# Kernel tuning notes

Hardware: AMD Instinct MI355X
Metric: run time of the kernel (lower is better)

## Reference

```python
import jax, jax.numpy as jnp
import numpy as np

H, D, E, C, F = 12, 64, 768, 512, 3072  # heads, kq_dim, emb_dim, context_dim, mlp_hid
EPS = 1e-5
SCALE = 1.0 / float(np.sqrt(D))


def setup_inputs() -> dict:
    key = jax.random.key(0)
    ks = jax.random.split(key, 12)
    rn = lambda k, s: jax.random.normal(k, s, dtype=jnp.float32) * 0.02
    z = lambda s: jnp.zeros(s, jnp.float32)
    o = lambda s: jnp.ones(s, jnp.float32)
    return {
        "emb": jax.random.normal(ks[0], (8, 1024, E), dtype=jnp.float32),
        "context": jax.random.normal(ks[1], (8, 256, C), dtype=jnp.float32),
        # self-attention (qkv_bias=False, value_up has bias)
        "sa_wq": rn(ks[2], (E, H * D)), "sa_wk": rn(ks[3], (E, H * D)),
        "sa_wv": rn(ks[4], (E, H * D)), "sa_wo": rn(ks[5], (H * D, E)), "sa_wo_b": z((E,)),
        "sa_qn_g": o((D,)), "sa_qn_b": z((D,)), "sa_kn_g": o((D,)), "sa_kn_b": z((D,)),
        # cross-attention
        "ca_wq": rn(ks[6], (E, H * D)), "ca_wk": rn(ks[7], (C, H * D)),
        "ca_wv": rn(ks[8], (C, H * D)), "ca_wo": rn(ks[9], (H * D, E)), "ca_wo_b": z((E,)),
        "ca_qn_g": o((D,)), "ca_qn_b": z((D,)), "ca_kn_g": o((D,)), "ca_kn_b": z((D,)),
        # MLP
        "mlp_w1": rn(ks[10], (E, F)), "mlp_b1": z((F,)),
        "mlp_w2": rn(ks[11], (F, E)), "mlp_b2": z((E,)),
        # block LayerNorms
        "ln1_g": o((E,)), "ln1_b": z((E,)),
        "ln2_g": o((E,)), "ln2_b": z((E,)),
        "ln3_g": o((E,)), "ln3_b": z((E,)),
    }


def _ln(x, g, b):
    m = jnp.mean(x, axis=-1, keepdims=True)
    v = jnp.mean(jnp.square(x - m), axis=-1, keepdims=True)
    return (x - m) / jnp.sqrt(v + EPS) * g + b


def _heads(x):  # [B,S,H*D] -> [B,H,S,D]
    B, S = x.shape[:2]
    return x.reshape(B, S, H, D).transpose(0, 2, 1, 3)


def _merge(x):  # [B,H,S,D] -> [B,S,H*D]
    B, h, S, d = x.shape
    return x.transpose(0, 2, 1, 3).reshape(B, S, h * d)


def _attn(qx, kvx, wq, wk, wv, wo, wo_b, qg, qb, kg, kb):
    q = _ln(_heads(qx @ wq), qg, qb)   # per-head QK-LayerNorm
    k = _ln(_heads(kvx @ wk), kg, kb)
    v = _heads(kvx @ wv)
    a = jax.nn.softmax(jnp.einsum('bhqd,bhkd->bhqk', q, k) * SCALE, axis=-1)
    return _merge(jnp.einsum('bhqk,bhkd->bhqd', a, v)) @ wo + wo_b


def reference(emb, context,
              sa_wq, sa_wk, sa_wv, sa_wo, sa_wo_b, sa_qn_g, sa_qn_b, sa_kn_g, sa_kn_b,
              ca_wq, ca_wk, ca_wv, ca_wo, ca_wo_b, ca_qn_g, ca_qn_b, ca_kn_g, ca_kn_b,
              mlp_w1, mlp_b1, mlp_w2, mlp_b2,
              ln1_g, ln1_b, ln2_g, ln2_b, ln3_g, ln3_b):
    # MultiHeadAttention.forward returns value + emb, and the block adds emb again
    sa = _attn(emb, emb, sa_wq, sa_wk, sa_wv, sa_wo, sa_wo_b,
               sa_qn_g, sa_qn_b, sa_kn_g, sa_kn_b)
    x = _ln(sa + emb + emb, ln1_g, ln1_b)  # faithful double residual
    ca = _attn(x, context, ca_wq, ca_wk, ca_wv, ca_wo, ca_wo_b,
               ca_qn_g, ca_qn_b, ca_kn_g, ca_kn_b)
    x = _ln(x + ca, ln2_g, ln2_b)
    x = jax.nn.gelu(x @ mlp_w1 + mlp_b1, approximate=False) @ mlp_w2 + mlp_b2
    return _ln(x, ln3_g, ln3_b)  # note: no residual around MLP in the original
```

## Files before the change

kernel.cpp:

```cpp
#include <hip/hip_runtime.h>
#include <hip/hip_bf16.h>
#include <math.h>

#define NH 12
#define HD 64
#define ED 768
#define CD 512
#define FD 3072
#define BB 8
#define SS 1024
#define TT 256
#define LN_EPS 1e-5f
#define ATT_SCALE 0.125f
#define QSC_LOG2E 0.1803368801111204f
#define P_M0 11.55f
#define TOT_R 6291456

typedef __attribute__((ext_vector_type(8))) __bf16 bf16x8;
typedef __attribute__((ext_vector_type(4))) __bf16 bf16x4;
typedef __attribute__((ext_vector_type(4))) float f32x4;

typedef const __attribute__((address_space(1))) void* gas1_t;
typedef __attribute__((address_space(3))) void* las3_t;

__device__ __forceinline__ void gl16(const void* g, void* l) {
  __builtin_amdgcn_global_load_lds((gas1_t)g, (las3_t)l, 16, 0, 0);
}

__device__ __forceinline__ ushort f2bf(float f) {
  union { __bf16 b; ushort u; } c;
  c.b = (__bf16)f;
  return c.u;
}
__device__ __forceinline__ float bf2f(ushort u) {
  return __uint_as_float((unsigned)u << 16);
}

__device__ __forceinline__ float gelu_fast(float c) {
  const float x2 = c * c;
  const float ex = __builtin_amdgcn_exp2f(c * (-2.3022084f - 0.10294325f * x2));
  return c * __builtin_amdgcn_rcpf(1.0f + ex);
}

__device__ __forceinline__ bf16x8 frag64(const ushort (*T)[64], int row, int q8) {
  return *(const bf16x8*)((const char*)T + row * 128 + ((q8 ^ (row & 7)) << 4));
}

struct CvtPack {
  const float* src[12];
  ushort* dst[12];
  int kd[12];
  int nd[12];
  int off[13];
};

__global__ __launch_bounds__(256) void cvt_all(CvtPack P) {
  __shared__ float t[32][33];
  const int flat = blockIdx.x;
  int j = 0;
  while (j < 11 && flat >= P.off[j + 1]) ++j;
  const int rel = flat - P.off[j];
  if (P.nd[j] == 0) {
    const int i = rel * 256 + threadIdx.x;
    if (i < P.kd[j]) {
      float4 v = ((const float4*)P.src[j])[i];
      ((ushort4*)P.dst[j])[i] =
          make_ushort4(f2bf(v.x), f2bf(v.y), f2bf(v.z), f2bf(v.w));
    }
    return;
  }
  const int Kd = P.kd[j], Nd = P.nd[j];
  const int ntx = Nd >> 5;
  const int n0 = (rel % ntx) * 32, k0 = (rel / ntx) * 32;
  const float* W = P.src[j];
  ushort* WT = P.dst[j];
  const int tx = threadIdx.x & 31, ty = threadIdx.x >> 5;
#pragma unroll
  for (int r = 0; r < 4; ++r)
    t[ty + 8 * r][tx] = W[(size_t)(k0 + ty + 8 * r) * Nd + n0 + tx];
  __syncthreads();
#pragma unroll
  for (int r = 0; r < 4; ++r)
    WT[(size_t)(n0 + ty + 8 * r) * Kd + k0 + tx] = f2bf(t[tx][ty + 8 * r]);
}

template <int MODE>
__global__ __launch_bounds__(256) void mfma_gemm(
    const ushort* __restrict__ A, const ushort* __restrict__ Wt,
    const float* __restrict__ bias, void* __restrict__ outp,
    int M, int N, int K, int sshift,
    const float* __restrict__ qg, const float* __restrict__ qb,
    const float* __restrict__ kg, const float* __restrict__ kb,
    int t_q, int t_k, int t_v) {
  __shared__ ushort As[2][128][64];
  __shared__ ushort Bs[2][128][64];
  const int tid = threadIdx.x;
  const int m0 = blockIdx.x * 128, n0 = blockIdx.y * 128;
  const int lane = tid & 63;
  const int wr = ((tid >> 6) >> 1) * 64, wc = ((tid >> 6) & 1) * 64;
  const int l15 = lane & 15, g = lane >> 4;
  f32x4 acc[4][4] = {};

  auto stage = [&](int bi, int kt) {
#pragma unroll
    for (int p = 0; p < 4; ++p) {
      const int flat = p * 256 + tid;
      const int row = flat >> 3, q8 = flat & 7;
      const int kc = 8 * (q8 ^ (row & 7));
      gl16(&A[(size_t)(m0 + row) * K + kt + kc], (char*)As[bi] + flat * 16);
      gl16(&Wt[(size_t)(n0 + row) * K + kt + kc], (char*)Bs[bi] + flat * 16);
    }
  };

  stage(0, 0);
  __syncthreads();
  int cur = 0;
  for (int kt = 0; kt < K; kt += 64) {
    if (kt + 64 < K) stage(cur ^ 1, kt + 64);
#pragma unroll
    for (int h = 0; h < 2; ++h) {
      bf16x8 af[4], bfv[4];
#pragma unroll
      for (int i = 0; i < 4; ++i) {
        af[i] = frag64(As[cur], wr + i * 16 + l15, 4 * h + g);
        bfv[i] = frag64(Bs[cur], wc + i * 16 + l15, 4 * h + g);
      }
#pragma unroll
      for (int i = 0; i < 4; ++i)
#pragma unroll
        for (int j = 0; j < 4; ++j)
          acc[i][j] = __builtin_amdgcn_mfma_f32_16x16x32_bf16(af[i], bfv[j],
                                                              acc[i][j], 0, 0, 0);
    }
    __syncthreads();
    cur ^= 1;
  }

  if (MODE == 2) {
    ushort* out = (ushort*)outp;
    const int Stok = 1 << sshift, smask = Stok - 1;
    const int ht0 = (n0 + wc) >> 6;
    const int t = ht0 / NH, h = ht0 - t * NH;
    const bool isq = (t == t_q), isk = (t == t_k);
    if (isq || isk) {
      const float* gg = isq ? qg : kg;
      const float* bb = isq ? qb : kb;
      const float osc = isq ? QSC_LOG2E : 1.0f;
      float gv[4], bv[4];
#pragma unroll
      for (int j = 0; j < 4; ++j) {
        gv[j] = gg[j * 16 + l15];
        bv[j] = bb[j * 16 + l15];
      }
#pragma unroll
      for (int i = 0; i < 4; ++i)
#pragma unroll
        for (int r = 0; r < 4; ++r) {
          float s = acc[i][0][r] + acc[i][1][r] + acc[i][2][r] + acc[i][3][r];
          float sq = acc[i][0][r] * acc[i][0][r] + acc[i][1][r] * acc[i][1][r] +
                     acc[i][2][r] * acc[i][2][r] + acc[i][3][r] * acc[i][3][r];
          s += __shfl_xor(s, 1);  sq += __shfl_xor(sq, 1);
          s += __shfl_xor(s, 2);  sq += __shfl_xor(sq, 2);
          s += __shfl_xor(s, 4);  sq += __shfl_xor(sq, 4);
          s += __shfl_xor(s, 8);  sq += __shfl_xor(sq, 8);
          const float mean = s * (1.0f / 64.0f);
          const float var = sq * (1.0f / 64.0f) - mean * mean;
          const float rs = rsqrtf(fmaxf(var, 0.0f) + LN_EPS);
#pragma unroll
          for (int j = 0; j < 4; ++j)
            acc[i][j][r] = ((acc[i][j][r] - mean) * rs * gv[j] + bv[j]) * osc;
        }
    }
    if (t == t_v) {
#pragma unroll
      for (int i = 0; i < 4; ++i) {
        const int row = m0 + wr + i * 16 + g * 4;
        const int b = row >> sshift, s2 = row & smask;
        ushort* obase =
            out + (size_t)t * TOT_R + (((size_t)b * NH + h) * 64) * Stok + s2;
#pragma unroll
        for (int j = 0; j < 4; ++j) {
          const int d = j * 16 + l15;
          ushort4 pk = make_ushort4(f2bf(acc[i][j][0]), f2bf(acc[i][j][1]),
                                    f2bf(acc[i][j][2]), f2bf(acc[i][j][3]));
          *(ushort4*)&obase[(size_t)d * Stok] = pk;
        }
      }
    } else {
#pragma unroll
      for (int i = 0; i < 4; ++i)
#pragma unroll
        for (int r = 0; r < 4; ++r) {
          const int row = m0 + wr + i * 16 + g * 4 + r;
          const int b = row >> sshift, s2 = row & smask;
          ushort* orow =
              out + (size_t)t * TOT_R + (((size_t)b * NH + h) * Stok + s2) * 64;
#pragma unroll
          for (int j = 0; j < 4; ++j) orow[j * 16 + l15] = f2bf(acc[i][j][r]);
        }
    }
  } else {
#pragma unroll
    for (int i = 0; i < 4; ++i) {
#pragma unroll
      for (int j = 0; j < 4; ++j) {
        const int gc = n0 + wc + j * 16 + l15;
        const float bv = bias ? bias[gc] : 0.0f;
#pragma unroll
        for (int r = 0; r < 4; ++r) {
          const int row = m0 + wr + i * 16 + g * 4 + r;
          float c = acc[i][j][r] + bv;
          if (MODE == 1) {
            c = gelu_fast(c);
            ((ushort*)outp)[(size_t)row * N + gc] = f2bf(c);
          } else if (MODE == 3) {
            ((ushort*)outp)[(size_t)row * N + gc] = f2bf(c);
          } else {
            ((float*)outp)[(size_t)row * N + gc] = c;
          }
        }
      }
    }
  }
}

__global__ __launch_bounds__(256) void mfma_gemm_ca(
    const ushort* __restrict__ A0, const ushort* __restrict__ Wt0,
    void* __restrict__ out0,
    const ushort* __restrict__ A1, const ushort* __restrict__ Wt1,
    void* __restrict__ out1,
    const float* __restrict__ qg, const float* __restrict__ qb,
    const float* __restrict__ kg, const float* __restrict__ kb) {
  __shared__ ushort As[2][128][64];
  __shared__ ushort Bs[2][128][64];
  const int tid = threadIdx.x;
  const int fb = blockIdx.x;
  const ushort* A;
  const ushort* Wt;
  ushort* out;
  int m0, n0, K, sshift, t_q, t_k, t_v;
  if (fb < 192) {
    A = A1; Wt = Wt1; out = (ushort*)out1;
    K = CD; sshift = 8;
    m0 = (fb & 15) * 128; n0 = (fb >> 4) * 128;
    t_q = -1; t_k = 0; t_v = 1;
  } else {
    const int id = fb - 192;
    A = A0; Wt = Wt0; out = (ushort*)out0;
    K = ED; sshift = 10;
    m0 = (id & 63) * 128; n0 = (id >> 6) * 128;
    t_q = 0; t_k = -1; t_v = -1;
  }
  const int lane = tid & 63;
  const int wr = ((tid >> 6) >> 1) * 64, wc = ((tid >> 6) & 1) * 64;
  const int l15 = lane & 15, g = lane >> 4;
  f32x4 acc[4][4] = {};

  auto stage = [&](int bi, int kt) {
#pragma unroll
    for (int p = 0; p < 4; ++p) {
      const int flat = p * 256 + tid;
      const int row = flat >> 3, q8 = flat & 7;
      const int kc = 8 * (q8 ^ (row & 7));
      gl16(&A[(size_t)(m0 + row) * K + kt + kc], (char*)As[bi] + flat * 16);
      gl16(&Wt[(size_t)(n0 + row) * K + kt + kc], (char*)Bs[bi] + flat * 16);
    }
  };

  stage(0, 0);
  __syncthreads();
  int cur = 0;
  for (int kt = 0; kt < K; kt += 64) {
    if (kt + 64 < K) stage(cur ^ 1, kt + 64);
#pragma unroll
    for (int h = 0; h < 2; ++h) {
      bf16x8 af[4], bfv[4];
#pragma unroll
      for (int i = 0; i < 4; ++i) {
        af[i] = frag64(As[cur], wr + i * 16 + l15, 4 * h + g);
        bfv[i] = frag64(Bs[cur], wc + i * 16 + l15, 4 * h + g);
      }
#pragma unroll
      for (int i = 0; i < 4; ++i)
#pragma unroll
        for (int j = 0; j < 4; ++j)
          acc[i][j] = __builtin_amdgcn_mfma_f32_16x16x32_bf16(af[i], bfv[j],
                                                              acc[i][j], 0, 0, 0);
    }
    __syncthreads();
    cur ^= 1;
  }

  const int Stok = 1 << sshift, smask = Stok - 1;
  const int ht0 = (n0 + wc) >> 6;
  const int t = ht0 / NH, h = ht0 - t * NH;
  const bool isq = (t == t_q), isk = (t == t_k);
  if (isq || isk) {
    const float* gg = isq ? qg : kg;
    const float* bb = isq ? qb : kb;
    const float osc = isq ? QSC_LOG2E : 1.0f;
    float gv[4], bv[4];
#pragma unroll
    for (int j = 0; j < 4; ++j) {
      gv[j] = gg[j * 16 + l15];
      bv[j] = bb[j * 16 + l15];
    }
#pragma unroll
    for (int i = 0; i < 4; ++i)
#pragma unroll
      for (int r = 0; r < 4; ++r) {
        float s = acc[i][0][r] + acc[i][1][r] + acc[i][2][r] + acc[i][3][r];
        float sq = acc[i][0][r] * acc[i][0][r] + acc[i][1][r] * acc[i][1][r] +
                   acc[i][2][r] * acc[i][2][r] + acc[i][3][r] * acc[i][3][r];
        s += __shfl_xor(s, 1);  sq += __shfl_xor(sq, 1);
        s += __shfl_xor(s, 2);  sq += __shfl_xor(sq, 2);
        s += __shfl_xor(s, 4);  sq += __shfl_xor(sq, 4);
        s += __shfl_xor(s, 8);  sq += __shfl_xor(sq, 8);
        const float mean = s * (1.0f / 64.0f);
        const float var = sq * (1.0f / 64.0f) - mean * mean;
        const float rs = rsqrtf(fmaxf(var, 0.0f) + LN_EPS);
#pragma unroll
        for (int j = 0; j < 4; ++j)
          acc[i][j][r] = ((acc[i][j][r] - mean) * rs * gv[j] + bv[j]) * osc;
      }
  }
  if (t == t_v) {
#pragma unroll
    for (int i = 0; i < 4; ++i) {
      const int row = m0 + wr + i * 16 + g * 4;
      const int b = row >> sshift, s2 = row & smask;
      ushort* obase =
          out + (size_t)t * TOT_R + (((size_t)b * NH + h) * 64) * Stok + s2;
#pragma unroll
      for (int j = 0; j < 4; ++j) {
        const int d = j * 16 + l15;
        ushort4 pk = make_ushort4(f2bf(acc[i][j][0]), f2bf(acc[i][j][1]),
                                  f2bf(acc[i][j][2]), f2bf(acc[i][j][3]));
        *(ushort4*)&obase[(size_t)d * Stok] = pk;
      }
    }
  } else {
#pragma unroll
    for (int i = 0; i < 4; ++i)
#pragma unroll
      for (int r = 0; r < 4; ++r) {
        const int row = m0 + wr + i * 16 + g * 4 + r;
        const int b = row >> sshift, s2 = row & smask;
        ushort* orow =
            out + (size_t)t * TOT_R + (((size_t)b * NH + h) * Stok + s2) * 64;
#pragma unroll
        for (int j = 0; j < 4; ++j) orow[j * 16 + l15] = f2bf(acc[i][j][r]);
      }
  }
}

__global__ __launch_bounds__(512) void flash_mfma(
    const ushort* __restrict__ Q, const ushort* __restrict__ K,
    const ushort* __restrict__ V, ushort* __restrict__ out, int Tkv) {
  __shared__ ushort Ks[2][64][64];
  __shared__ ushort Vt[2][80][64];
  __shared__ ushort Ps[8][16][64];
  const int bh = blockIdx.x;
  const int b = bh / NH, h = bh % NH;
  const int qt = blockIdx.y;
  const int tid = threadIdx.x;
  const int w = tid >> 6, lane = tid & 63;
  const int l15 = lane & 15, g = lane >> 4;
  const int srow = tid >> 3;
  const int q8s = tid & 7;
  const int skc = 8 * (q8s ^ (srow & 7));
  const int kperm = 4 * (srow & 15) + (srow >> 4);

  const ushort* Qb = Q + ((size_t)bh * SS + qt * 256) * 64;
  const ushort* Kb = K + (size_t)bh * Tkv * 64;
  const ushort* Vb = V + (size_t)bh * Tkv * 64;

  gl16(&Kb[(size_t)kperm * 64 + skc], (char*)Ks[0] + tid * 16);
  gl16(&Vb[(size_t)srow * Tkv + skc], (char*)Vt[0] + tid * 16);

  if (tid < 256) {
    const int bi = tid >> 7, rq = tid & 127;
    const uint4 ov = make_uint4(0x3F803F80u, 0x3F803F80u, 0x3F803F80u, 0x3F803F80u);
    *(uint4*)((char*)Vt[bi] + (64 + (rq >> 3)) * 128 + ((rq & 7) << 4)) = ov;
  }

  const ushort* qr0 = Qb + (w * 32 + l15) * 64;
  const bf16x8 qf00 = *(const bf16x8*)&qr0[g * 8];
  const bf16x8 qf01 = *(const bf16x8*)&qr0[32 + g * 8];
  const bf16x8 qf10 = *(const bf16x8*)&qr0[16 * 64 + g * 8];
  const bf16x8 qf11 = *(const bf16x8*)&qr0[16 * 64 + 32 + g * 8];
  __syncthreads();

  f32x4 oa[2][5] = {};
  const int pwofs = ((((l15 >> 1) ^ ((g * 4) & 7)) << 4) | ((l15 & 1) << 3));

  const int nch = Tkv >> 6;
  int cur = 0;
  for (int ci = 0; ci < nch; ++ci) {
    if (ci + 1 < nch) {
      const int cnx = (ci + 1) << 6;
      const int nxt = cur ^ 1;
      gl16(&Kb[(size_t)(cnx + kperm) * 64 + skc], (char*)Ks[nxt] + tid * 16);
      gl16(&Vb[(size_t)srow * Tkv + cnx + skc], (char*)Vt[nxt] + tid * 16);
    }

    f32x4 s[2][4] = {};
    __builtin_amdgcn_s_setprio(1);
#pragma unroll
    for (int kb = 0; kb < 4; ++kb) {
      bf16x8 kf0 = frag64(Ks[cur], kb * 16 + l15, g);
      bf16x8 kf1 = frag64(Ks[cur], kb * 16 + l15, 4 + g);
      s[0][kb] = __builtin_amdgcn_mfma_f32_16x16x32_bf16(qf00, kf0, s[0][kb], 0, 0, 0);
      s[0][kb] = __builtin_amdgcn_mfma_f32_16x16x32_bf16(qf01, kf1, s[0][kb], 0, 0, 0);
      s[1][kb] = __builtin_amdgcn_mfma_f32_16x16x32_bf16(qf10, kf0, s[1][kb], 0, 0, 0);
      s[1][kb] = __builtin_amdgcn_mfma_f32_16x16x32_bf16(qf11, kf1, s[1][kb], 0, 0, 0);
    }
    __builtin_amdgcn_s_setprio(0);

    bf16x8 pfr[2][2];
#pragma unroll
    for (int sub = 0; sub < 2; ++sub) {
#pragma unroll
      for (int r = 0; r < 4; ++r) {
        bf16x4 pk;
#pragma unroll
        for (int kbv = 0; kbv < 4; ++kbv)
          pk[kbv] = (__bf16)__builtin_amdgcn_exp2f(s[sub][kbv][r] - P_M0);
        *(bf16x4*)((char*)Ps[w] + (g * 4 + r) * 128 + (pwofs ^ ((r & 7) << 4))) = pk;
      }
      pfr[sub][0] = frag64(Ps[w], l15, g);
      pfr[sub][1] = frag64(Ps[w], l15, 4 + g);
    }

    __builtin_amdgcn_s_setprio(1);
#pragma unroll
    for (int jd = 0; jd < 5; ++jd) {
      const int d = jd * 16 + l15;
      bf16x8 vf0 = frag64(Vt[cur], d, g);
      bf16x8 vf1 = frag64(Vt[cur], d, 4 + g);
      oa[0][jd] = __builtin_amdgcn_mfma_f32_16x16x32_bf16(pfr[0][0], vf0, oa[0][jd], 0, 0, 0);
      oa[0][jd] = __builtin_amdgcn_mfma_f32_16x16x32_bf16(pfr[0][1], vf1, oa[0][jd], 0, 0, 0);
      oa[1][jd] = __builtin_amdgcn_mfma_f32_16x16x32_bf16(pfr[1][0], vf0, oa[1][jd], 0, 0, 0);
      oa[1][jd] = __builtin_amdgcn_mfma_f32_16x16x32_bf16(pfr[1][1], vf1, oa[1][jd], 0, 0, 0);
    }
    __builtin_amdgcn_s_setprio(0);

    __syncthreads();
    cur ^= 1;
  }

#pragma unroll
  for (int sub = 0; sub < 2; ++sub)
#pragma unroll
    for (int r = 0; r < 4; ++r) {
      const int row = qt * 256 + w * 32 + sub * 16 + g * 4 + r;
      const float inv = 1.0f / oa[sub][4][r];
#pragma unroll
      for (int jd = 0; jd < 4; ++jd)
        out[((size_t)b * SS + row) * ED + h * 64 + jd * 16 + l15] =
            f2bf(oa[sub][jd][r] * inv);
    }
}

__global__ __launch_bounds__(256) void add_ln(
    const float* __restrict__ af, const ushort* __restrict__ ab,
    const float* __restrict__ bsrc, float alpha,
    const float* __restrict__ g, const float* __restrict__ bt,
    float* __restrict__ outf, ushort* __restrict__ outb) {
  const int row = blockIdx.x * 4 + (threadIdx.x >> 6);
  const int lane = threadIdx.x & 63;
  const size_t base = (size_t)row * ED;
  float4 x[3];
#pragma unroll
  for (int p = 0; p < 3; ++p) {
    const int idx = p * 256 + lane * 4;
    if (af) {
      x[p] = *(const float4*)&af[base + idx];
    } else {
      ushort4 u = *(const ushort4*)&ab[base + idx];
      x[p] = make_float4(bf2f(u.x), bf2f(u.y), bf2f(u.z), bf2f(u.w));
    }
    if (bsrc) {
      float4 bv = *(const float4*)&bsrc[base + idx];
      x[p].x += alpha * bv.x;
      x[p].y += alpha * bv.y;
      x[p].z += alpha * bv.z;
      x[p].w += alpha * bv.w;
    }
  }
  float s = 0.f;
#pragma unroll
  for (int p = 0; p < 3; ++p) s += x[p].x + x[p].y + x[p].z + x[p].w;
  for (int off = 32; off; off >>= 1) s += __shfl_xor(s, off);
  const float mean = s * (1.0f / 768.0f);
  float v = 0.f;
#pragma unroll
  for (int p = 0; p < 3; ++p) {
    float d0 = x[p].x - mean, d1 = x[p].y - mean;
    float d2 = x[p].z - mean, d3 = x[p].w - mean;
    v += d0 * d0 + d1 * d1 + d2 * d2 + d3 * d3;
  }
  for (int off = 32; off; off >>= 1) v += __shfl_xor(v, off);
  const float rs = rsqrtf(v * (1.0f / 768.0f) + LN_EPS);
#pragma unroll
  for (int p = 0; p < 3; ++p) {
    const int idx = p * 256 + lane * 4;
    const float4 gv = *(const float4*)&g[idx];
    const float4 bb = *(const float4*)&bt[idx];
    const float y0 = (x[p].x - mean) * rs * gv.x + bb.x;
    const float y1 = (x[p].y - mean) * rs * gv.y + bb.y;
    const float y2 = (x[p].z - mean) * rs * gv.z + bb.z;
    const float y3 = (x[p].w - mean) * rs * gv.w + bb.w;
    if (outf) *(float4*)&outf[base + idx] = make_float4(y0, y1, y2, y3);
    if (outb)
      *(ushort4*)&outb[base + idx] =
          make_ushort4(f2bf(y0), f2bf(y1), f2bf(y2), f2bf(y3));
  }
}

extern "C" void kernel_launch(void* const* d_in, const int* in_sizes, int n_in,
                              void* d_out, int out_size, void* d_ws,
                              size_t ws_size, hipStream_t stream) {
  (void)in_sizes; (void)n_in; (void)out_size; (void)ws_size;
  const float* emb     = (const float*)d_in[0];
  const float* context = (const float*)d_in[1];
  const float* sa_wq = (const float*)d_in[2];
  const float* sa_wk = (const float*)d_in[3];
  const float* sa_wv = (const float*)d_in[4];
  const float* sa_wo = (const float*)d_in[5];
  const float* sa_wo_b = (const float*)d_in[6];
  const float* sa_qn_g = (const float*)d_in[7];
  const float* sa_qn_b = (const float*)d_in[8];
  const float* sa_kn_g = (const float*)d_in[9];
  const float* sa_kn_b = (const float*)d_in[10];
  const float* ca_wq = (const float*)d_in[11];
  const float* ca_wk = (const float*)d_in[12];
  const float* ca_wv = (const float*)d_in[13];
  const float* ca_wo = (const float*)d_in[14];
  const float* ca_wo_b = (const float*)d_in[15];
  const float* ca_qn_g = (const float*)d_in[16];
  const float* ca_qn_b = (const float*)d_in[17];
  const float* ca_kn_g = (const float*)d_in[18];
  const float* ca_kn_b = (const float*)d_in[19];
  const float* mlp_w1 = (const float*)d_in[20];
  const float* mlp_b1 = (const float*)d_in[21];
  const float* mlp_w2 = (const float*)d_in[22];
  const float* mlp_b2 = (const float*)d_in[23];
  const float* ln1_g = (const float*)d_in[24];
  const float* ln1_b = (const float*)d_in[25];
  const float* ln2_g = (const float*)d_in[26];
  const float* ln2_b = (const float*)d_in[27];
  const float* ln3_g = (const float*)d_in[28];
  const float* ln3_b = (const float*)d_in[29];
  float* out = (float*)d_out;

  const size_t R = TOT_R;
  ushort* U = (ushort*)d_ws;
  ushort* Qh  = U;
  ushort* Kh  = U + R;
  ushort* Vh  = U + 2 * R;
  ushort* SH1 = U + 3 * R;
  ushort* SH2 = U + 4 * R;
  ushort* WB  = U + 5 * R;
  float*  X1  = (float*)(U + 5 * R + 9043968);
  ushort* WOb = Qh;
  ushort* M2b = (ushort*)X1;
  ushort* Hb  = Qh;

  ushort* w_saqkv = WB;
  ushort* w_sao   = WB + 1769472;
  ushort* w_caq   = WB + 2359296;
  ushort* w_cakv  = WB + 2949120;
  ushort* w_cao   = WB + 3735552;
  ushort* w_m1    = WB + 4325376;
  ushort* w_m2    = WB + 6684672;

  dim3 blk(256);

  CvtPack P;
  const float* srcs[12] = {sa_wq, sa_wk, sa_wv, sa_wo, ca_wq, ca_wk, ca_wv,
                           ca_wo, mlp_w1, mlp_w2, emb, context};
  ushort* dsts[12] = {w_saqkv, w_saqkv + 589824, w_saqkv + 1179648, w_sao,
                      w_caq, w_cakv, w_cakv + 393216, w_cao, w_m1, w_m2,
                      SH1, SH2};
  const int kds[12] = {ED, ED, ED, ED, ED, CD, CD, ED, ED, FD,
                       1572864, 262144};
  const int nds[12] = {ED, ED, ED, ED, ED, ED, ED, ED, FD, ED, 0, 0};
  int off = 0;
  for (int j = 0; j < 12; ++j) {
    P.src[j] = srcs[j]; P.dst[j] = dsts[j]; P.kd[j] = kds[j]; P.nd[j] = nds[j];
    P.off[j] = off;
    off += nds[j] ? (nds[j] >> 5) * (kds[j] >> 5) : (kds[j] + 255) >> 8;
  }
  P.off[12] = off;
  cvt_all<<<dim3(off), blk, 0, stream>>>(P);

  mfma_gemm<2><<<dim3(64, 18), blk, 0, stream>>>(
      SH1, w_saqkv, nullptr, Qh, 8192, 2304, ED, 10,
      sa_qn_g, sa_qn_b, sa_kn_g, sa_kn_b, 0, 1, 2);
  flash_mfma<<<dim3(96, 4), dim3(512), 0, stream>>>(Qh, Kh, Vh, SH1, SS);
  mfma_gemm<3><<<dim3(64, 6), blk, 0, stream>>>(
      SH1, w_sao, sa_wo_b, WOb, 8192, ED, ED, 0,
      nullptr, nullptr, nullptr, nullptr, -1, -1, -1);
  add_ln<<<dim3(2048), blk, 0, stream>>>(nullptr, WOb, emb, 2.0f,
                                         ln1_g, ln1_b, X1, SH1);

  mfma_gemm_ca<<<dim3(576), blk, 0, stream>>>(
      SH1, w_caq, Qh, SH2, w_cakv, Kh,
      ca_qn_g, ca_qn_b, ca_kn_g, ca_kn_b);
  flash_mfma<<<dim3(96, 4), dim3(512), 0, stream>>>(Qh, Kh, Vh, SH1, TT);
  mfma_gemm<3><<<dim3(64, 6), blk, 0, stream>>>(
      SH1, w_cao, ca_wo_b, WOb, 8192, ED, ED, 0,
      nullptr, nullptr, nullptr, nullptr, -1, -1, -1);
  add_ln<<<dim3(2048), blk, 0, stream>>>(nullptr, WOb, X1, 1.0f,
                                         ln2_g, ln2_b, nullptr, SH2);

  mfma_gemm<1><<<dim3(64, 24), blk, 0, stream>>>(
      SH2, w_m1, mlp_b1, Hb, 8192, FD, ED, 0,
      nullptr, nullptr, nullptr, nullptr, -1, -1, -1);
  mfma_gemm<3><<<dim3(64, 6), blk, 0, stream>>>(
      Hb, w_m2, mlp_b2, M2b, 8192, ED, FD, 0,
      nullptr, nullptr, nullptr, nullptr, -1, -1, -1);
  add_ln<<<dim3(2048), blk, 0, stream>>>(nullptr, M2b, nullptr, 0.0f,
                                         ln3_g, ln3_b, out, nullptr);
}
```

Measured before the change: 334.3 us.

## Use 256x256-tile triple-buffered 8-wave GEMM kernel for MLP up-projection

Adds a dedicated GEMM kernel for the MLP first layer (8192x3072x768 with GELU). It uses 256x256 output tiles, 512 threads and a 3-stage LDS pipeline with BK=32, and interleaves async global-to-LDS loads with MFMA phases under s_setprio. Larger tiles raise arithmetic intensity and cut global traffic per FLOP, and deeper buffering hides load latency. In exchange it uses more registers (128 accumulators per lane) and launches only 384 blocks, which may hurt occupancy or tail balance.

```diff
diff --git a/kernel.cpp b/kernel.cpp
--- a/kernel.cpp
+++ b/kernel.cpp
@@ -44,6 +44,10 @@
 
 __device__ __forceinline__ bf16x8 frag64(const ushort (*T)[64], int row, int q8) {
   return *(const bf16x8*)((const char*)T + row * 128 + ((q8 ^ (row & 7)) << 4));
+}
+
+__device__ __forceinline__ bf16x8 frag32(const ushort (*T)[32], int row, int g) {
+  return *(const bf16x8*)((const char*)T + row * 64 + ((g ^ ((row >> 1) & 3)) << 4));
 }
 
 struct CvtPack {
@@ -219,6 +223,91 @@
             ((float*)outp)[(size_t)row * N + gc] = c;
           }
         }
+      }
+    }
+  }
+}
+
+__global__ __launch_bounds__(512, 2) void mfma_gemm8(
+    const ushort* __restrict__ A, const ushort* __restrict__ Wt,
+    const float* __restrict__ bias, ushort* __restrict__ outp, int N, int K) {
+  __shared__ ushort As[3][256][32];
+  __shared__ ushort Bs[3][256][32];
+  const int tid = threadIdx.x;
+  const int m0 = blockIdx.x * 256, n0 = blockIdx.y * 256;
+  const int lane = tid & 63;
+  const int w = tid >> 6;
+  const int wm = w >> 2, wn = w & 3;
+  const int l15 = lane & 15, g = lane >> 4;
+  const int rbase = wm * 128;
+  const int cbase = wn * 64;
+  f32x4 acc[8][4] = {};
+
+  auto stagec = [&](int bi, int kt, int c) {
+    const int fq = (c & 1) * 512 + tid;
+    const int row = fq >> 2, q = fq & 3;
+    const int kc = 8 * (q ^ ((row >> 1) & 3));
+    if (c < 2)
+      gl16(&A[(size_t)(m0 + row) * K + kt + kc], (char*)As[bi] + fq * 16);
+    else
+      gl16(&Wt[(size_t)(n0 + row) * K + kt + kc], (char*)Bs[bi] + fq * 16);
+  };
+
+  const int nst = K >> 5;
+#pragma unroll
+  for (int c = 0; c < 4; ++c) stagec(0, 0, c);
+#pragma unroll
+  for (int c = 0; c < 4; ++c) stagec(1, 32, c);
+
+  int bt = 0;
+  for (int t = 0; t < nst; ++t) {
+    if (t < nst - 1) asm volatile("s_waitcnt vmcnt(4)" ::: "memory");
+    else             asm volatile("s_waitcnt vmcnt(0)" ::: "memory");
+    __builtin_amdgcn_s_barrier();
+    int b2 = bt + 2; if (b2 >= 3) b2 -= 3;
+    const bool pf = (t + 2 < nst);
+    const int kt2 = (t + 2) * 32;
+
+    bf16x8 af[8], bf[4];
+#pragma unroll
+    for (int i = 0; i < 8; ++i) af[i] = frag32(As[bt], rbase + i * 16 + l15, g);
+    bf[0] = frag32(Bs[bt], cbase + l15, g);
+    bf[1] = frag32(Bs[bt], cbase + 16 + l15, g);
+    if (pf) { stagec(b2, kt2, 0); stagec(b2, kt2, 1); }
+    __builtin_amdgcn_s_barrier();
+    __builtin_amdgcn_s_setprio(1);
+#pragma unroll
+    for (int i = 0; i < 8; ++i) {
+      acc[i][0] = __builtin_amdgcn_mfma_f32_16x16x32_bf16(af[i], bf[0], acc[i][0], 0, 0, 0);
+      acc[i][1] = __builtin_amdgcn_mfma_f32_16x16x32_bf16(af[i], bf[1], acc[i][1], 0, 0, 0);
+    }
+    __builtin_amdgcn_s_setprio(0);
+    __builtin_amdgcn_s_barrier();
+    bf[2] = frag32(Bs[bt], cbase + 32 + l15, g);
+    bf[3] = frag32(Bs[bt], cbase + 48 + l15, g);
+    if (pf) { stagec(b2, kt2, 2); stagec(b2, kt2, 3); }
+    __builtin_amdgcn_s_barrier();
+    __builtin_amdgcn_s_setprio(1);
+#pragma unroll
+    for (int i = 0; i < 8; ++i) {
+      acc[i][2] = __builtin_amdgcn_mfma_f32_16x16x32_bf16(af[i], bf[2], acc[i][2], 0, 0, 0);
+      acc[i][3] = __builtin_amdgcn_mfma_f32_16x16x32_bf16(af[i], bf[3], acc[i][3], 0, 0, 0);
+    }
+    __builtin_amdgcn_s_setprio(0);
+    __builtin_amdgcn_s_barrier();
+    if (++bt == 3) bt = 0;
+  }
+
+#pragma unroll
+  for (int i = 0; i < 8; ++i) {
+#pragma unroll
+    for (int j = 0; j < 4; ++j) {
+      const int gc = n0 + cbase + j * 16 + l15;
+      const float bv = bias[gc];
+#pragma unroll
+      for (int r = 0; r < 4; ++r) {
+        const int row = m0 + rbase + i * 16 + g * 4 + r;
+        outp[(size_t)row * N + gc] = f2bf(gelu_fast(acc[i][j][r] + bv));
       }
     }
   }
@@ -615,9 +704,8 @@
   add_ln<<<dim3(2048), blk, 0, stream>>>(nullptr, WOb, X1, 1.0f,
                                          ln2_g, ln2_b, nullptr, SH2);
 
-  mfma_gemm<1><<<dim3(64, 24), blk, 0, stream>>>(
-      SH2, w_m1, mlp_b1, Hb, 8192, FD, ED, 0,
-      nullptr, nullptr, nullptr, nullptr, -1, -1, -1);
+  mfma_gemm8<<<dim3(32, 12), dim3(512), 0, stream>>>(
+      SH2, w_m1, mlp_b1, Hb, FD, ED);
   mfma_gemm<3><<<dim3(64, 6), blk, 0, stream>>>(
       Hb, w_m2, mlp_b2, M2b, 8192, ED, FD, 0,
       nullptr, nullptr, nullptr, nullptr, -1, -1, -1);
```

New measurement: 334.5 us. About the same (+0.0%).
